# Performance work log

Hardware: AMD Instinct MI355X
Metric: run time of the kernel (lower is better)

Reference implementation:

```python
import jax, jax.numpy as jnp
import numpy as np

KH, KW, STRIDE, PAD = 3, 3, 1, 1


def unfold(img, kh, kw, stride, padding):
    # torch.nn.functional.unfold, transposed to [B, L, C*kh*kw] with (c, kh, kw)-major ordering
    b, c, h, w = img.shape
    p = jnp.pad(img, ((0, 0), (0, 0), (padding, padding), (padding, padding)))
    oh = (h - kh + 2 * padding) // stride + 1
    ow = (w - kw + 2 * padding) // stride + 1
    # [b, c, kh*kw, oh, ow]; static python loop over the 9 kernel offsets only
    cols = jnp.stack([p[:, :, i:i + oh * stride:stride, j:j + ow * stride:stride]
                      for i in range(kh) for j in range(kw)], axis=2)
    return cols.reshape(b, c * kh * kw, oh * ow).transpose(0, 2, 1), oh, ow


def setup_inputs() -> dict:
    key = jax.random.key(0)
    k1, k2 = jax.random.split(key)
    img = jax.random.normal(k1, (8, 64, 112, 112), dtype=jnp.float32)
    weights = 0.8 * jax.random.normal(k2, (64, 64, 3, 3), dtype=jnp.float32)
    return {"img": img, "weights": weights}


def reference(img, weights):
    b = img.shape[0]
    O = weights.shape[0]
    W = weights.reshape(O, -1)            # [O, K], K = in_ch*kh*kw
    K = W.shape[1]
    u, oh, ow = unfold(img, KH, KW, STRIDE, PAD)   # [b, L, K]
    u2 = u * u
    u3 = u2 * u

    def gemm(poly):
        return jnp.einsum('blk,ok->blo', poly, W)

    # f: identity-kernel term has all-zero coefficients (p00=p10=p20=p30=0) -> drops out
    f = gemm(-0.000287 + 0.266 * u - 0.1097 * u2) / 75

    # identity_kernel is all ones, so (const*ones) @ ones.T == const * K (scalar)
    g1 = (0.11 / 75) * K + gemm(0.001309 + 0.00619 * u - 0.009 * u2 + 0.001383 * u3)
    g2 = (0.179 / 75) * K + gemm(-0.0025 + 0.00303 * u - 0.00484 * u2 + 0.0175 * u3)
    g3 = (0.238 / 75) * K + gemm(-0.000954 + 0.00187 * u + 0.001877 * u2 + 0.01502 * u3)
    g4 = (0.388 / 75) * K + gemm(-0.00734 + 0.001117 * u + 0.00752 * u2 + 0.009 * u3)
    g5 = (0.507 / 75) * K + gemm(-0.01017 + 0.000426 * u + 0.00837 * u2 + 0.00413 * u3)

    sig = jax.nn.sigmoid
    s1 = sig(10 * (0.15 - f))
    s2 = sig(10 * (f - 0.15)) + sig(10 * (0.23 - f)) - 1
    s3 = sig(10 * (f - 0.23)) + sig(10 * (0.32 - f)) - 1
    s4 = sig(10 * (f - 0.32)) + sig(10 * (0.39 - f)) - 1
    s5 = sig(10 * (f - 0.39))

    out = s1 * g1 + s2 * g2 + s3 * g3 + s4 * g4 + s5 * g5   # [b, L, O]
    return out.transpose(0, 2, 1).reshape(b, O, oh, ow)
```

## Files before the change

kernel.cpp:

```cpp
#include <hip/hip_runtime.h>

#define HW   112
#define PH   114
#define KK   576
#define ROWB (PH * 128)
#define PLANE_SH (8 * PH * PH * 64)
#define PLANE_B  (PLANE_SH * 2)
#define WB_OFF_SH (3 * PLANE_SH)
#define S_OFF_SH  (WB_OFF_SH + 36864)

typedef __attribute__((ext_vector_type(8))) short s16x8;
typedef __attribute__((ext_vector_type(4))) float f32x4;
typedef __attribute__((ext_vector_type(2))) float f32x2;
typedef __attribute__((address_space(3))) unsigned int lds_u32;
typedef const __attribute__((address_space(1))) unsigned int glb_u32;

__device__ inline unsigned short f2bf(float f) {
    unsigned u = __float_as_uint(f);
    u += 0x7FFF + ((u >> 16) & 1);
    return (unsigned short)(u >> 16);
}

__global__ __launch_bounds__(256) void prep_pow(const float* __restrict__ img,
                                                const float* __restrict__ W,
                                                unsigned short* __restrict__ pw,
                                                unsigned short* __restrict__ wb,
                                                float* __restrict__ S) {
    __shared__ __align__(16) unsigned short sA[3 * 112 * 72];
    const int bid = blockIdx.x, t = threadIdx.x;
    if (bid < 896) {
        const int b = bid / 112, y = bid - b * 112;
        const int c = t & 63, xq0 = t >> 6;
        const float4* src = (const float4*)(img + (((size_t)(b * 64 + c) * HW + y) * HW));
        #pragma unroll
        for (int i = 0; i < 7; ++i) {
            const int xq = xq0 + i * 4;
            const float4 v = src[xq];
            const float vv[4] = {v.x, v.y, v.z, v.w};
            #pragma unroll
            for (int u = 0; u < 4; ++u) {
                const float v1 = vv[u], v2 = v1 * v1, v3 = v2 * v1;
                const int x = xq * 4 + u;
                sA[x * 72 + c]         = f2bf(v1);
                sA[8064 + x * 72 + c]  = f2bf(v2);
                sA[16128 + x * 72 + c] = f2bf(v3);
            }
        }
        __syncthreads();
        for (int i = 0; i < 11; ++i) {
            const int ch = t + i * 256;
            if (ch >= 2688) break;
            const int p = ch / 896, r = ch - p * 896;
            const int x = r >> 3, c8 = r & 7;
            const s16x8 val = *(const s16x8*)&sA[p * 8064 + x * 72 + c8 * 8];
            *(s16x8*)&pw[(size_t)p * PLANE_SH + ((size_t)(b * PH + y + 1) * PH + (x + 1)) * 64 + c8 * 8] = val;
        }
    } else if (bid < 920) {
        const int k = bid - 896;
        const int p = k >> 3, b = k & 7;
        unsigned short* base = pw + (size_t)p * PLANE_SH + (size_t)b * PH * PH * 64;
        const s16x8 z = {0, 0, 0, 0, 0, 0, 0, 0};
        for (int i = 0; i < 15; ++i) {
            const int e = t + i * 256;
            if (e >= 3616) break;
            const int n = e >> 3, c8 = e & 7;
            int x, yy;
            if (n < 114)      { yy = 0;   x = n; }
            else if (n < 228) { yy = 113; x = n - 114; }
            else { const int m2 = n - 228; yy = 1 + (m2 >> 1); x = (m2 & 1) ? 113 : 0; }
            *(s16x8*)&base[(yy * PH + x) * 64 + c8 * 8] = z;
        }
    } else if (bid < 1064) {
        const int i   = (bid - 920) * 256 + t;
        const int j   = i & 7;
        const int l   = (i >> 3) & 63;
        const int nt  = (i >> 9) & 3;
        const int cc  = (i >> 11) & 1;
        const int tap = i >> 12;
        const int c   = cc * 32 + ((l >> 4) << 3) + j;
        const int o   = nt * 16 + (l & 15);
        wb[i] = f2bf(W[o * KK + c * 9 + tap]);
    } else {
        __shared__ float partial[256];
        const int o = t >> 2, part = t & 3;
        const float4* row = (const float4*)(W + o * KK) + part * 36;
        float s = 0.f;
        for (int k = 0; k < 36; ++k) { float4 v = row[k]; s += v.x + v.y + v.z + v.w; }
        partial[t] = s;
        __syncthreads();
        if (part == 0) S[o] = partial[t] + partial[t + 1] + partial[t + 2] + partial[t + 3];
    }
}

#define LP_PLANE 11520
#define LP_ROW   1152
#define STAGE_B  34560
#define WH_B     18432

__global__ __launch_bounds__(256, 3) void conv_main(const unsigned short* __restrict__ pw,
                                                    const unsigned short* __restrict__ wb,
                                                    const float* __restrict__ S,
                                                    float* __restrict__ out) {
    __shared__ __align__(16) char ldsw[WH_B];
    __shared__ __align__(16) char tile[STAGE_B];

    const int t = threadIdx.x, wv = t >> 6, lane = t & 63;
    const int m = lane & 15, q = lane >> 4;

    const int bid = blockIdx.x;
    const int b = bid & 7;
    const int rest = bid >> 3;
    const int oc2 = rest & 1;
    const int r = rest >> 1;
    const int ty = r / 7, tx = r - ty * 7;
    const int y0 = ty * 8, x0 = tx * 16;

    f32x4 acc[3][2][2];
    #pragma unroll
    for (int p = 0; p < 3; ++p)
        #pragma unroll
        for (int at = 0; at < 2; ++at)
            #pragma unroll
            for (int ntl = 0; ntl < 2; ++ntl)
                acc[p][at][ntl] = (f32x4){0.f, 0.f, 0.f, 0.f};

    const char* pwin = (const char*)pw + ((size_t)(b * PH + y0) * PH + x0) * 128;

    #pragma unroll 1
    for (int cc = 0; cc < 2; ++cc) {
        if (cc) __syncthreads();
        #pragma unroll
        for (int i = 0; i < 5; ++i) {
            const int f = i * 4096 + t * 16;
            if (f < WH_B) {
                const int lchunk = f >> 10;
                const int tap = lchunk >> 1, ntl = lchunk & 1;
                const char* gp = (const char*)wb
                    + ((size_t)((tap * 2 + cc) * 4 + oc2 * 2 + ntl)) * 1024 + lane * 16;
                lds_u32* lp = (lds_u32*)(ldsw + i * 4096 + wv * 1024);
                __builtin_amdgcn_global_load_lds((glb_u32*)gp, lp, 16, 0, 0);
            }
        }
        #pragma unroll
        for (int i = 0; i < 9; ++i) {
            const int f = i * 4096 + t * 16;
            if (f < STAGE_B) {
                const int p   = f / LP_PLANE;
                const int r1  = f - p * LP_PLANE;
                const int row = r1 / LP_ROW;
                const int r2  = r1 - row * LP_ROW;
                const int px  = r2 >> 6;
                const int c8s = (r2 >> 4) & 3;
                const int c8  = c8s ^ (px & 3) ^ ((px >> 2) & 3);
                const char* gp = pwin + (size_t)p * PLANE_B + row * ROWB + px * 128 + cc * 64 + c8 * 16;
                lds_u32* lp = (lds_u32*)(tile + i * 4096 + wv * 1024);
                __builtin_amdgcn_global_load_lds((glb_u32*)gp, lp, 16, 0, 0);
            }
        }
        __syncthreads();

        #pragma unroll
        for (int kx = 0; kx < 3; ++kx) {
            s16x8 bf[3][2];
            #pragma unroll
            for (int ky = 0; ky < 3; ++ky)
                #pragma unroll
                for (int ntl = 0; ntl < 2; ++ntl)
                    bf[ky][ntl] = *(const s16x8*)&ldsw[(((ky * 3 + kx) * 2 + ntl) << 10) + lane * 16];
            const int pxr  = m + kx;
            const int c8sr = q ^ (pxr & 3) ^ ((pxr >> 2) & 3);
            const int abase = wv * (2 * LP_ROW) + pxr * 64 + c8sr * 16;
            s16x8 af[4][3];
            #pragma unroll
            for (int r4 = 0; r4 < 4; ++r4)
                #pragma unroll
                for (int p = 0; p < 3; ++p)
                    af[r4][p] = *(const s16x8*)&tile[abase + r4 * LP_ROW + p * LP_PLANE];
            #pragma unroll
            for (int ky = 0; ky < 3; ++ky)
                #pragma unroll
                for (int at = 0; at < 2; ++at)
                    #pragma unroll
                    for (int p = 0; p < 3; ++p)
                        #pragma unroll
                        for (int ntl = 0; ntl < 2; ++ntl)
                            acc[p][at][ntl] = __builtin_amdgcn_mfma_f32_16x16x32_bf16(
                                af[at + ky][p], bf[ky][ntl], acc[p][at][ntl], 0, 0, 0);
        }
    }

    #pragma unroll
    for (int ntl = 0; ntl < 2; ++ntl) {
        const int o = (oc2 * 2 + ntl) * 16 + (lane & 15);
        const float Sv = S[o];
        const float fS = -0.000287f / 75.f * Sv;
        const float cg1 = 0.8448f  + 0.001309f * Sv;
        const float D1  = 0.52992f - 0.003809f * Sv;
        const float D2  = 0.45312f + 0.001546f * Sv;
        const float D3  = 1.152f   - 0.006386f * Sv;
        const float D4  = 0.91392f - 0.00283f  * Sv;
        #pragma unroll
        for (int at = 0; at < 2; ++at) {
            float res[4];
            #pragma unroll
            for (int h = 0; h < 2; ++h) {
                const f32x2 u1 = {acc[0][at][ntl][2 * h], acc[0][at][ntl][2 * h + 1]};
                const f32x2 u2 = {acc[1][at][ntl][2 * h], acc[1][at][ntl][2 * h + 1]};
                const f32x2 u3 = {acc[2][at][ntl][2 * h], acc[2][at][ntl][2 * h + 1]};
                const f32x2 f  = fS   + 0.00354667f * u1 - 0.00146267f * u2;
                const f32x2 g1 = cg1  + 0.00619f    * u1 - 0.009f      * u2 + 0.001383f * u3;
                const f32x2 d1 = D1   - 0.00316f    * u1 + 0.00416f    * u2 + 0.016117f * u3;
                const f32x2 d2 = D2   - 0.00116f    * u1 + 0.006717f   * u2 - 0.00248f  * u3;
                const f32x2 d3 = D3   - 0.000753f   * u1 + 0.005643f   * u2 - 0.00602f  * u3;
                const f32x2 d4 = D4   - 0.000691f   * u1 + 0.00085f    * u2 - 0.00487f  * u3;
                f32x2 E;
                E.x = __expf(-10.f * f.x);
                E.y = __expf(-10.f * f.y);
                const f32x2 den1 = 1.f + E * 4.4816890703f;
                const f32x2 den2 = 1.f + E * 9.9741824548f;
                const f32x2 den3 = 1.f + E * 24.5325301971f;
                const f32x2 den4 = 1.f + E * 49.4024491055f;
                f32x2 o2 = g1;
                o2.x += __builtin_amdgcn_rcpf(den1.x) * d1.x + __builtin_amdgcn_rcpf(den2.x) * d2.x
                      + __builtin_amdgcn_rcpf(den3.x) * d3.x + __builtin_amdgcn_rcpf(den4.x) * d4.x;
                o2.y += __builtin_amdgcn_rcpf(den1.y) * d1.y + __builtin_amdgcn_rcpf(den2.y) * d2.y
                      + __builtin_amdgcn_rcpf(den3.y) * d3.y + __builtin_amdgcn_rcpf(den4.y) * d4.y;
                res[2 * h] = o2.x; res[2 * h + 1] = o2.y;
            }
            const int y = y0 + 2 * wv + at;
            float* op = out + (((size_t)(b * 64 + o)) * HW + y) * HW + x0 + q * 4;
            *(float4*)op = make_float4(res[0], res[1], res[2], res[3]);
        }
    }
}

extern "C" void kernel_launch(void* const* d_in, const int* in_sizes, int n_in,
                              void* d_out, int out_size, void* d_ws, size_t ws_size,
                              hipStream_t stream) {
    const float* img = (const float*)d_in[0];
    const float* w   = (const float*)d_in[1];
    float* outp = (float*)d_out;
    unsigned short* pw = (unsigned short*)d_ws;
    unsigned short* wb = pw + WB_OFF_SH;
    float* S = (float*)(pw + S_OFF_SH);

    hipLaunchKernelGGL(prep_pow,  dim3(1065), dim3(256), 0, stream, img, w, pw, wb, S);
    hipLaunchKernelGGL(conv_main, dim3(1568), dim3(256), 0, stream, pw, wb, S, outp);
}
```

Before: 110.9 us.

## Double-buffer activation planes in LDS and keep weights in registers

Splits the LDS staging of the three power planes into six phases (plane × channel chunk) that cycle through a two-buffer ring. Loads for the next phase are issued while MFMAs run on the current one, with explicit vmcnt waits and barriers. Weights are now read straight from global memory into registers instead of staged through LDS, and MFMA blocks get raised wave priority. LDS use drops, which may allow more resident blocks, but holding 18 weight vectors in registers raises VGPR pressure and the extra barriers add sync cost.

```diff
diff --git a/kernel.cpp b/kernel.cpp
--- a/kernel.cpp
+++ b/kernel.cpp
@@ -92,17 +92,14 @@
     }
 }
 
-#define LP_PLANE 11520
 #define LP_ROW   1152
-#define STAGE_B  34560
-#define WH_B     18432
+#define LP_PHASE 11520
 
 __global__ __launch_bounds__(256, 3) void conv_main(const unsigned short* __restrict__ pw,
                                                     const unsigned short* __restrict__ wb,
                                                     const float* __restrict__ S,
                                                     float* __restrict__ out) {
-    __shared__ __align__(16) char ldsw[WH_B];
-    __shared__ __align__(16) char tile[STAGE_B];
+    __shared__ __align__(16) char tile[2 * LP_PHASE];
 
     const int t = threadIdx.x, wv = t >> 6, lane = t & 63;
     const int m = lane & 15, q = lane >> 4;
@@ -124,69 +121,87 @@
             for (int ntl = 0; ntl < 2; ++ntl)
                 acc[p][at][ntl] = (f32x4){0.f, 0.f, 0.f, 0.f};
 
-    const char* pwin = (const char*)pw + ((size_t)(b * PH + y0) * PH + x0) * 128;
-
-    #pragma unroll 1
-    for (int cc = 0; cc < 2; ++cc) {
-        if (cc) __syncthreads();
-        #pragma unroll
-        for (int i = 0; i < 5; ++i) {
+    const char* pwin  = (const char*)pw + ((size_t)(b * PH + y0) * PH + x0) * 128;
+    const char* wbase = (const char*)wb + oc2 * 2048 + lane * 16;
+
+    s16x8 bfr[9][2];
+
+    auto loadW = [&](int cc) {
+        #pragma unroll
+        for (int tap = 0; tap < 9; ++tap)
+            #pragma unroll
+            for (int ntl = 0; ntl < 2; ++ntl)
+                bfr[tap][ntl] = *(const s16x8*)(wbase + (tap * 2 + cc) * 4096 + ntl * 1024);
+    };
+
+    auto stageA = [&](int cc, int p, int buf) {
+        #pragma unroll
+        for (int i = 0; i < 3; ++i) {
             const int f = i * 4096 + t * 16;
-            if (f < WH_B) {
-                const int lchunk = f >> 10;
-                const int tap = lchunk >> 1, ntl = lchunk & 1;
-                const char* gp = (const char*)wb
-                    + ((size_t)((tap * 2 + cc) * 4 + oc2 * 2 + ntl)) * 1024 + lane * 16;
-                lds_u32* lp = (lds_u32*)(ldsw + i * 4096 + wv * 1024);
-                __builtin_amdgcn_global_load_lds((glb_u32*)gp, lp, 16, 0, 0);
-            }
-        }
-        #pragma unroll
-        for (int i = 0; i < 9; ++i) {
-            const int f = i * 4096 + t * 16;
-            if (f < STAGE_B) {
-                const int p   = f / LP_PLANE;
-                const int r1  = f - p * LP_PLANE;
-                const int row = r1 / LP_ROW;
-                const int r2  = r1 - row * LP_ROW;
+            if (f < LP_PHASE) {
+                const int row = f / LP_ROW;
+                const int r2  = f - row * LP_ROW;
                 const int px  = r2 >> 6;
                 const int c8s = (r2 >> 4) & 3;
                 const int c8  = c8s ^ (px & 3) ^ ((px >> 2) & 3);
                 const char* gp = pwin + (size_t)p * PLANE_B + row * ROWB + px * 128 + cc * 64 + c8 * 16;
-                lds_u32* lp = (lds_u32*)(tile + i * 4096 + wv * 1024);
+                lds_u32* lp = (lds_u32*)(tile + buf * LP_PHASE + i * 4096 + wv * 1024);
                 __builtin_amdgcn_global_load_lds((glb_u32*)gp, lp, 16, 0, 0);
             }
         }
-        __syncthreads();
-
+    };
+
+    loadW(0);
+    __builtin_amdgcn_sched_barrier(0);
+    stageA(0, 0, 0);
+    stageA(0, 1, 1);
+    __builtin_amdgcn_sched_barrier(0);
+
+    #pragma unroll
+    for (int pb = 0; pb < 6; ++pb) {
+        const int p   = (pb < 3) ? pb : pb - 3;
+        const int buf = pb & 1;
+
+        if (pb < 5) asm volatile("s_waitcnt vmcnt(3)" ::: "memory");
+        else        asm volatile("s_waitcnt vmcnt(0)" ::: "memory");
+        __builtin_amdgcn_sched_barrier(0);
+        __builtin_amdgcn_s_barrier();
+        __builtin_amdgcn_sched_barrier(0);
+
+        const char* base = tile + buf * LP_PHASE;
         #pragma unroll
         for (int kx = 0; kx < 3; ++kx) {
-            s16x8 bf[3][2];
-            #pragma unroll
-            for (int ky = 0; ky < 3; ++ky)
-                #pragma unroll
-                for (int ntl = 0; ntl < 2; ++ntl)
-                    bf[ky][ntl] = *(const s16x8*)&ldsw[(((ky * 3 + kx) * 2 + ntl) << 10) + lane * 16];
             const int pxr  = m + kx;
             const int c8sr = q ^ (pxr & 3) ^ ((pxr >> 2) & 3);
             const int abase = wv * (2 * LP_ROW) + pxr * 64 + c8sr * 16;
-            s16x8 af[4][3];
+            s16x8 af[4];
             #pragma unroll
             for (int r4 = 0; r4 < 4; ++r4)
-                #pragma unroll
-                for (int p = 0; p < 3; ++p)
-                    af[r4][p] = *(const s16x8*)&tile[abase + r4 * LP_ROW + p * LP_PLANE];
+                af[r4] = *(const s16x8*)&base[abase + r4 * LP_ROW];
+            __builtin_amdgcn_s_setprio(1);
             #pragma unroll
             for (int ky = 0; ky < 3; ++ky)
                 #pragma unroll
                 for (int at = 0; at < 2; ++at)
                     #pragma unroll
-                    for (int p = 0; p < 3; ++p)
-                        #pragma unroll
-                        for (int ntl = 0; ntl < 2; ++ntl)
-                            acc[p][at][ntl] = __builtin_amdgcn_mfma_f32_16x16x32_bf16(
-                                af[at + ky][p], bf[ky][ntl], acc[p][at][ntl], 0, 0, 0);
-        }
+                    for (int ntl = 0; ntl < 2; ++ntl)
+                        acc[p][at][ntl] = __builtin_amdgcn_mfma_f32_16x16x32_bf16(
+                            af[at + ky], bfr[ky * 3 + kx][ntl], acc[p][at][ntl], 0, 0, 0);
+            __builtin_amdgcn_s_setprio(0);
+        }
+
+        __builtin_amdgcn_sched_barrier(0);
+        __builtin_amdgcn_s_barrier();
+        __builtin_amdgcn_sched_barrier(0);
+        if (pb == 2) {
+            loadW(1);
+            __builtin_amdgcn_sched_barrier(0);
+        }
+        if (pb < 4) {
+            const int pn = pb + 2;
+            stageA((pn < 3) ? 0 : 1, (pn < 3) ? pn : pn - 3, buf);
+        }
+        __builtin_amdgcn_sched_barrier(0);
     }
 
     #pragma unroll
```

After: 109.7 us. Within noise of the previous version (-1.1%).

## Fuse power-plane preparation into conv kernel and keep weights in registers

Applied to the files above, without the earlier changes.

Drops the separate pass that wrote padded bf16 u, u², u³ planes to global memory. Each conv block now reads fp32 image rows directly, computes the powers, converts them to bf16 and writes them into a swizzled LDS tile, handling halo padding inline. Weight fragments are loaded straight into registers instead of being staged in LDS, and the MFMA loop is reordered by power plane with setprio around it. This removes a large intermediate global write and read plus one heavy prep launch. In exchange the conv kernel does redundant halo loads and scalar LDS stores from only 160 threads, and register pressure goes up.

```diff
diff --git a/kernel.cpp b/kernel.cpp
--- a/kernel.cpp
+++ b/kernel.cpp
@@ -1,77 +1,31 @@
 #include <hip/hip_runtime.h>
 
 #define HW   112
-#define PH   114
 #define KK   576
-#define ROWB (PH * 128)
-#define PLANE_SH (8 * PH * PH * 64)
-#define PLANE_B  (PLANE_SH * 2)
-#define WB_OFF_SH (3 * PLANE_SH)
-#define S_OFF_SH  (WB_OFF_SH + 36864)
 
 typedef __attribute__((ext_vector_type(8))) short s16x8;
 typedef __attribute__((ext_vector_type(4))) float f32x4;
 typedef __attribute__((ext_vector_type(2))) float f32x2;
-typedef __attribute__((address_space(3))) unsigned int lds_u32;
-typedef const __attribute__((address_space(1))) unsigned int glb_u32;
+
+#define LP_ROW   1184
+#define LP_PHASE (10 * LP_ROW)
+#define SWZ(px)  (((px) & 3) ^ (((px) >> 2) & 3))
 
 __device__ inline unsigned short f2bf(float f) {
     unsigned u = __float_as_uint(f);
     u += 0x7FFF + ((u >> 16) & 1);
     return (unsigned short)(u >> 16);
 }
-
-__global__ __launch_bounds__(256) void prep_pow(const float* __restrict__ img,
-                                                const float* __restrict__ W,
-                                                unsigned short* __restrict__ pw,
-                                                unsigned short* __restrict__ wb,
-                                                float* __restrict__ S) {
-    __shared__ __align__(16) unsigned short sA[3 * 112 * 72];
+__device__ inline unsigned pack2(float lo, float hi) {
+    return (unsigned)f2bf(lo) | ((unsigned)f2bf(hi) << 16);
+}
+
+__global__ __launch_bounds__(256) void prep_w(const float* __restrict__ W,
+                                              unsigned short* __restrict__ wb,
+                                              float* __restrict__ S) {
     const int bid = blockIdx.x, t = threadIdx.x;
-    if (bid < 896) {
-        const int b = bid / 112, y = bid - b * 112;
-        const int c = t & 63, xq0 = t >> 6;
-        const float4* src = (const float4*)(img + (((size_t)(b * 64 + c) * HW + y) * HW));
-        #pragma unroll
-        for (int i = 0; i < 7; ++i) {
-            const int xq = xq0 + i * 4;
-            const float4 v = src[xq];
-            const float vv[4] = {v.x, v.y, v.z, v.w};
-            #pragma unroll
-            for (int u = 0; u < 4; ++u) {
-                const float v1 = vv[u], v2 = v1 * v1, v3 = v2 * v1;
-                const int x = xq * 4 + u;
-                sA[x * 72 + c]         = f2bf(v1);
-                sA[8064 + x * 72 + c]  = f2bf(v2);
-                sA[16128 + x * 72 + c] = f2bf(v3);
-            }
-        }
-        __syncthreads();
-        for (int i = 0; i < 11; ++i) {
-            const int ch = t + i * 256;
-            if (ch >= 2688) break;
-            const int p = ch / 896, r = ch - p * 896;
-            const int x = r >> 3, c8 = r & 7;
-            const s16x8 val = *(const s16x8*)&sA[p * 8064 + x * 72 + c8 * 8];
-            *(s16x8*)&pw[(size_t)p * PLANE_SH + ((size_t)(b * PH + y + 1) * PH + (x + 1)) * 64 + c8 * 8] = val;
-        }
-    } else if (bid < 920) {
-        const int k = bid - 896;
-        const int p = k >> 3, b = k & 7;
-        unsigned short* base = pw + (size_t)p * PLANE_SH + (size_t)b * PH * PH * 64;
-        const s16x8 z = {0, 0, 0, 0, 0, 0, 0, 0};
-        for (int i = 0; i < 15; ++i) {
-            const int e = t + i * 256;
-            if (e >= 3616) break;
-            const int n = e >> 3, c8 = e & 7;
-            int x, yy;
-            if (n < 114)      { yy = 0;   x = n; }
-            else if (n < 228) { yy = 113; x = n - 114; }
-            else { const int m2 = n - 228; yy = 1 + (m2 >> 1); x = (m2 & 1) ? 113 : 0; }
-            *(s16x8*)&base[(yy * PH + x) * 64 + c8 * 8] = z;
-        }
-    } else if (bid < 1064) {
-        const int i   = (bid - 920) * 256 + t;
+    if (bid < 144) {
+        const int i   = bid * 256 + t;
         const int j   = i & 7;
         const int l   = (i >> 3) & 63;
         const int nt  = (i >> 9) & 3;
@@ -92,17 +46,11 @@
     }
 }
 
-#define LP_PLANE 11520
-#define LP_ROW   1152
-#define STAGE_B  34560
-#define WH_B     18432
-
-__global__ __launch_bounds__(256, 3) void conv_main(const unsigned short* __restrict__ pw,
-                                                    const unsigned short* __restrict__ wb,
-                                                    const float* __restrict__ S,
-                                                    float* __restrict__ out) {
-    __shared__ __align__(16) char ldsw[WH_B];
-    __shared__ __align__(16) char tile[STAGE_B];
+__global__ __launch_bounds__(256, 3) void conv_fused(const float* __restrict__ img,
+                                                     const unsigned short* __restrict__ wb,
+                                                     const float* __restrict__ S,
+                                                     float* __restrict__ out) {
+    __shared__ __align__(16) char tile[3 * LP_PHASE];
 
     const int t = threadIdx.x, wv = t >> 6, lane = t & 63;
     const int m = lane & 15, q = lane >> 4;
@@ -124,68 +72,82 @@
             for (int ntl = 0; ntl < 2; ++ntl)
                 acc[p][at][ntl] = (f32x4){0.f, 0.f, 0.f, 0.f};
 
-    const char* pwin = (const char*)pw + ((size_t)(b * PH + y0) * PH + x0) * 128;
+    const char* wbase = (const char*)wb + oc2 * 2048 + lane * 16;
+    s16x8 bfr[9][2];
 
     #pragma unroll 1
     for (int cc = 0; cc < 2; ++cc) {
         if (cc) __syncthreads();
-        #pragma unroll
-        for (int i = 0; i < 5; ++i) {
-            const int f = i * 4096 + t * 16;
-            if (f < WH_B) {
-                const int lchunk = f >> 10;
-                const int tap = lchunk >> 1, ntl = lchunk & 1;
-                const char* gp = (const char*)wb
-                    + ((size_t)((tap * 2 + cc) * 4 + oc2 * 2 + ntl)) * 1024 + lane * 16;
-                lds_u32* lp = (lds_u32*)(ldsw + i * 4096 + wv * 1024);
-                __builtin_amdgcn_global_load_lds((glb_u32*)gp, lp, 16, 0, 0);
+
+        if (t < 160) {
+            const int cp = t & 15, row = t >> 4;
+            const int y = y0 + row - 1;
+            float va[2][18];
+            if (y < 0 || y >= HW) {
+                #pragma unroll
+                for (int e = 0; e < 2; ++e)
+                    #pragma unroll
+                    for (int px = 0; px < 18; ++px) va[e][px] = 0.f;
+            } else {
+                #pragma unroll
+                for (int e = 0; e < 2; ++e) {
+                    const float* rp = img + ((size_t)(b * 64 + cc * 32 + cp * 2 + e) * HW + y) * HW;
+                    va[e][0] = (x0 > 0) ? rp[x0 - 1] : 0.f;
+                    #pragma unroll
+                    for (int i2 = 0; i2 < 4; ++i2) {
+                        const float4 v = *(const float4*)(rp + x0 + i2 * 4);
+                        va[e][1 + 4 * i2] = v.x;
+                        va[e][2 + 4 * i2] = v.y;
+                        va[e][3 + 4 * i2] = v.z;
+                        va[e][4 + 4 * i2] = v.w;
+                    }
+                    va[e][17] = (x0 + 16 < HW) ? rp[x0 + 16] : 0.f;
+                }
+            }
+            char* wp = tile + row * LP_ROW + (cp & 3) * 4;
+            #pragma unroll
+            for (int px = 0; px < 18; ++px) {
+                char* a0 = wp + px * 64 + (((cp >> 2) ^ SWZ(px)) << 4);
+                const float l1 = va[0][px], h1 = va[1][px];
+                const float l2 = l1 * l1,   h2 = h1 * h1;
+                const float l3 = l2 * l1,   h3 = h2 * h1;
+                *(unsigned*)(a0)                = pack2(l1, h1);
+                *(unsigned*)(a0 + LP_PHASE)     = pack2(l2, h2);
+                *(unsigned*)(a0 + 2 * LP_PHASE) = pack2(l3, h3);
             }
         }
-        #pragma unroll
-        for (int i = 0; i < 9; ++i) {
-            const int f = i * 4096 + t * 16;
-            if (f < STAGE_B) {
-                const int p   = f / LP_PLANE;
-                const int r1  = f - p * LP_PLANE;
-                const int row = r1 / LP_ROW;
-                const int r2  = r1 - row * LP_ROW;
-                const int px  = r2 >> 6;
-                const int c8s = (r2 >> 4) & 3;
-                const int c8  = c8s ^ (px & 3) ^ ((px >> 2) & 3);
-                const char* gp = pwin + (size_t)p * PLANE_B + row * ROWB + px * 128 + cc * 64 + c8 * 16;
-                lds_u32* lp = (lds_u32*)(tile + i * 4096 + wv * 1024);
-                __builtin_amdgcn_global_load_lds((glb_u32*)gp, lp, 16, 0, 0);
-            }
-        }
+
+        #pragma unroll
+        for (int tap = 0; tap < 9; ++tap)
+            #pragma unroll
+            for (int ntl = 0; ntl < 2; ++ntl)
+                bfr[tap][ntl] = *(const s16x8*)(wbase + (tap * 2 + cc) * 4096 + ntl * 1024);
+
         __syncthreads();
 
         #pragma unroll
-        for (int kx = 0; kx < 3; ++kx) {
-            s16x8 bf[3][2];
-            #pragma unroll
-            for (int ky = 0; ky < 3; ++ky)
-                #pragma unroll
-                for (int ntl = 0; ntl < 2; ++ntl)
-                    bf[ky][ntl] = *(const s16x8*)&ldsw[(((ky * 3 + kx) * 2 + ntl) << 10) + lane * 16];
-            const int pxr  = m + kx;
-            const int c8sr = q ^ (pxr & 3) ^ ((pxr >> 2) & 3);
-            const int abase = wv * (2 * LP_ROW) + pxr * 64 + c8sr * 16;
-            s16x8 af[4][3];
-            #pragma unroll
-            for (int r4 = 0; r4 < 4; ++r4)
-                #pragma unroll
-                for (int p = 0; p < 3; ++p)
-                    af[r4][p] = *(const s16x8*)&tile[abase + r4 * LP_ROW + p * LP_PLANE];
-            #pragma unroll
-            for (int ky = 0; ky < 3; ++ky)
-                #pragma unroll
-                for (int at = 0; at < 2; ++at)
+        for (int p = 0; p < 3; ++p) {
+            const char* base = tile + p * LP_PHASE;
+            #pragma unroll
+            for (int kx = 0; kx < 3; ++kx) {
+                const int pxr  = m + kx;
+                const int c8sr = q ^ SWZ(pxr);
+                const int abase = wv * (2 * LP_ROW) + pxr * 64 + c8sr * 16;
+                s16x8 af[4];
+                #pragma unroll
+                for (int r4 = 0; r4 < 4; ++r4)
+                    af[r4] = *(const s16x8*)&base[abase + r4 * LP_ROW];
+                __builtin_amdgcn_s_setprio(1);
+                #pragma unroll
+                for (int ky = 0; ky < 3; ++ky)
                     #pragma unroll
-                    for (int p = 0; p < 3; ++p)
+                    for (int at = 0; at < 2; ++at)
                         #pragma unroll
                         for (int ntl = 0; ntl < 2; ++ntl)
                             acc[p][at][ntl] = __builtin_amdgcn_mfma_f32_16x16x32_bf16(
-                                af[at + ky][p], bf[ky][ntl], acc[p][at][ntl], 0, 0, 0);
+                                af[at + ky], bfr[ky * 3 + kx][ntl], acc[p][at][ntl], 0, 0, 0);
+                __builtin_amdgcn_s_setprio(0);
+            }
         }
     }
 
@@ -240,10 +202,9 @@
     const float* img = (const float*)d_in[0];
     const float* w   = (const float*)d_in[1];
     float* outp = (float*)d_out;
-    unsigned short* pw = (unsigned short*)d_ws;
-    unsigned short* wb = pw + WB_OFF_SH;
-    float* S = (float*)(pw + S_OFF_SH);
-
-    hipLaunchKernelGGL(prep_pow,  dim3(1065), dim3(256), 0, stream, img, w, pw, wb, S);
-    hipLaunchKernelGGL(conv_main, dim3(1568), dim3(256), 0, stream, pw, wb, S, outp);
-}
+    unsigned short* wb = (unsigned short*)d_ws;
+    float* S = (float*)(wb + 36864);
+
+    hipLaunchKernelGGL(prep_w,     dim3(145),  dim3(256), 0, stream, w, wb, S);
+    hipLaunchKernelGGL(conv_fused, dim3(1568), dim3(256), 0, stream, img, wb, S, outp);
+}
```

Measured after the change: 109.8 us. Within noise of the previous version (-1.0%).

## Replace LDS staging with direct global-to-register fragment loads in conv kernel

Applied to the files above, without the earlier changes.

The main conv kernel no longer stages weights and the input tile through LDS with global_load_lds and barriers. Each wave now loads its MFMA A and B fragments straight from global memory into registers, keeping all 9 taps of weights in registers per channel chunk, and occupancy is lowered to 2 blocks per SM. This removes LDS traffic and synchronisation. The cost is redundant global/L2 loads across waves, since the overlapping 3x3 halo rows are re-read, plus higher register pressure.

```diff
diff --git a/kernel.cpp b/kernel.cpp
--- a/kernel.cpp
+++ b/kernel.cpp
@@ -12,8 +12,6 @@
 typedef __attribute__((ext_vector_type(8))) short s16x8;
 typedef __attribute__((ext_vector_type(4))) float f32x4;
 typedef __attribute__((ext_vector_type(2))) float f32x2;
-typedef __attribute__((address_space(3))) unsigned int lds_u32;
-typedef const __attribute__((address_space(1))) unsigned int glb_u32;
 
 __device__ inline unsigned short f2bf(float f) {
     unsigned u = __float_as_uint(f);
@@ -92,18 +90,10 @@
     }
 }
 
-#define LP_PLANE 11520
-#define LP_ROW   1152
-#define STAGE_B  34560
-#define WH_B     18432
-
-__global__ __launch_bounds__(256, 3) void conv_main(const unsigned short* __restrict__ pw,
-                                                    const unsigned short* __restrict__ wb,
-                                                    const float* __restrict__ S,
-                                                    float* __restrict__ out) {
-    __shared__ __align__(16) char ldsw[WH_B];
-    __shared__ __align__(16) char tile[STAGE_B];
-
+__global__ __launch_bounds__(256, 2) void conv_reg(const unsigned short* __restrict__ pw,
+                                                   const unsigned short* __restrict__ wb,
+                                                   const float* __restrict__ S,
+                                                   float* __restrict__ out) {
     const int t = threadIdx.x, wv = t >> 6, lane = t & 63;
     const int m = lane & 15, q = lane >> 4;
 
@@ -124,68 +114,38 @@
             for (int ntl = 0; ntl < 2; ++ntl)
                 acc[p][at][ntl] = (f32x4){0.f, 0.f, 0.f, 0.f};
 
-    const char* pwin = (const char*)pw + ((size_t)(b * PH + y0) * PH + x0) * 128;
-
-    #pragma unroll 1
+    const char* wbase  = (const char*)wb + oc2 * 2048 + lane * 16;
+    const char* abase0 = (const char*)pw
+        + ((size_t)(b * PH + y0 + 2 * wv) * PH + (x0 + m)) * 128 + q * 16;
+
+    s16x8 bfr[9][2];
+
+    #pragma unroll
     for (int cc = 0; cc < 2; ++cc) {
-        if (cc) __syncthreads();
-        #pragma unroll
-        for (int i = 0; i < 5; ++i) {
-            const int f = i * 4096 + t * 16;
-            if (f < WH_B) {
-                const int lchunk = f >> 10;
-                const int tap = lchunk >> 1, ntl = lchunk & 1;
-                const char* gp = (const char*)wb
-                    + ((size_t)((tap * 2 + cc) * 4 + oc2 * 2 + ntl)) * 1024 + lane * 16;
-                lds_u32* lp = (lds_u32*)(ldsw + i * 4096 + wv * 1024);
-                __builtin_amdgcn_global_load_lds((glb_u32*)gp, lp, 16, 0, 0);
-            }
-        }
-        #pragma unroll
-        for (int i = 0; i < 9; ++i) {
-            const int f = i * 4096 + t * 16;
-            if (f < STAGE_B) {
-                const int p   = f / LP_PLANE;
-                const int r1  = f - p * LP_PLANE;
-                const int row = r1 / LP_ROW;
-                const int r2  = r1 - row * LP_ROW;
-                const int px  = r2 >> 6;
-                const int c8s = (r2 >> 4) & 3;
-                const int c8  = c8s ^ (px & 3) ^ ((px >> 2) & 3);
-                const char* gp = pwin + (size_t)p * PLANE_B + row * ROWB + px * 128 + cc * 64 + c8 * 16;
-                lds_u32* lp = (lds_u32*)(tile + i * 4096 + wv * 1024);
-                __builtin_amdgcn_global_load_lds((glb_u32*)gp, lp, 16, 0, 0);
-            }
-        }
-        __syncthreads();
+        #pragma unroll
+        for (int tap = 0; tap < 9; ++tap)
+            #pragma unroll
+            for (int ntl = 0; ntl < 2; ++ntl)
+                bfr[tap][ntl] = *(const s16x8*)(wbase + (tap * 2 + cc) * 4096 + ntl * 1024);
 
         #pragma unroll
         for (int kx = 0; kx < 3; ++kx) {
-            s16x8 bf[3][2];
-            #pragma unroll
-            for (int ky = 0; ky < 3; ++ky)
+            #pragma unroll
+            for (int p = 0; p < 3; ++p) {
+                const char* ab = abase0 + (size_t)p * PLANE_B + cc * 64 + kx * 128;
+                s16x8 af[4];
                 #pragma unroll
-                for (int ntl = 0; ntl < 2; ++ntl)
-                    bf[ky][ntl] = *(const s16x8*)&ldsw[(((ky * 3 + kx) * 2 + ntl) << 10) + lane * 16];
-            const int pxr  = m + kx;
-            const int c8sr = q ^ (pxr & 3) ^ ((pxr >> 2) & 3);
-            const int abase = wv * (2 * LP_ROW) + pxr * 64 + c8sr * 16;
-            s16x8 af[4][3];
-            #pragma unroll
-            for (int r4 = 0; r4 < 4; ++r4)
+                for (int r4 = 0; r4 < 4; ++r4)
+                    af[r4] = *(const s16x8*)(ab + r4 * ROWB);
                 #pragma unroll
-                for (int p = 0; p < 3; ++p)
-                    af[r4][p] = *(const s16x8*)&tile[abase + r4 * LP_ROW + p * LP_PLANE];
-            #pragma unroll
-            for (int ky = 0; ky < 3; ++ky)
-                #pragma unroll
-                for (int at = 0; at < 2; ++at)
+                for (int ky = 0; ky < 3; ++ky)
                     #pragma unroll
-                    for (int p = 0; p < 3; ++p)
+                    for (int at = 0; at < 2; ++at)
                         #pragma unroll
                         for (int ntl = 0; ntl < 2; ++ntl)
                             acc[p][at][ntl] = __builtin_amdgcn_mfma_f32_16x16x32_bf16(
-                                af[at + ky][p], bf[ky][ntl], acc[p][at][ntl], 0, 0, 0);
+                                af[at + ky], bfr[ky * 3 + kx][ntl], acc[p][at][ntl], 0, 0, 0);
+            }
         }
     }
 
@@ -244,6 +204,6 @@
     unsigned short* wb = pw + WB_OFF_SH;
     float* S = (float*)(pw + S_OFF_SH);
 
-    hipLaunchKernelGGL(prep_pow,  dim3(1065), dim3(256), 0, stream, img, w, pw, wb, S);
-    hipLaunchKernelGGL(conv_main, dim3(1568), dim3(256), 0, stream, pw, wb, S, outp);
-}
+    hipLaunchKernelGGL(prep_pow, dim3(1065), dim3(256), 0, stream, img, w, pw, wb, S);
+    hipLaunchKernelGGL(conv_reg, dim3(1568), dim3(256), 0, stream, pw, wb, S, outp);
+}
```

New measurement: 151.8 us. 1.37x slower.
